# Kernel optimization log

Measured on AMD Instinct MI355X. Metric: run time of the kernel, lower is better.

Reference implementation:

```python
import jax, jax.numpy as jnp
import numpy as np

H = 1024
NH = 16
HD = H // NH
EPS = 1e-5

def setup_inputs() -> dict:
    key = jax.random.key(0)
    ks = jax.random.split(key, 5)
    B, S = 2, 2048
    scale = 1.0 / np.sqrt(H)
    return {
        "x": jax.random.normal(ks[0], (B, S, H), dtype=jnp.float32),
        "Wq": jax.random.normal(ks[1], (H, H), dtype=jnp.float32) * scale,
        "Wk": jax.random.normal(ks[2], (H, H), dtype=jnp.float32) * scale,
        "Wv": jax.random.normal(ks[3], (H, H), dtype=jnp.float32) * scale,
        "Wo": jax.random.normal(ks[4], (H, H), dtype=jnp.float32) * scale,
        "bo": jnp.zeros((H,), dtype=jnp.float32),
        "gamma": jnp.ones((H,), dtype=jnp.float32),
        "beta": jnp.zeros((H,), dtype=jnp.float32),
    }

def reference(x, Wq, Wk, Wv, Wo, bo, gamma, beta):
    B, S, _ = x.shape
    residual = x
    # pre-LayerNorm
    mu = jnp.mean(x, axis=-1, keepdims=True)
    var = jnp.mean(jnp.square(x - mu), axis=-1, keepdims=True)
    xn = (x - mu) * jax.lax.rsqrt(var + EPS) * gamma + beta
    # QKV projections (torch Linear: y = x @ W.T), split heads -> [B, NH, S, HD]
    q = (xn @ Wq.T).reshape(B, S, NH, HD).transpose(0, 2, 1, 3)
    k = (xn @ Wk.T).reshape(B, S, NH, HD).transpose(0, 2, 1, 3)
    v = (xn @ Wv.T).reshape(B, S, NH, HD).transpose(0, 2, 1, 3)
    # naive attention: explicit [B, NH, S, S] scores
    scale = 1.0 / np.sqrt(HD)
    scores = jnp.einsum('bhqd,bhkd->bhqk', q, k) * scale
    attn = jax.nn.softmax(scores.astype(jnp.float32), axis=-1).astype(q.dtype)
    out = jnp.einsum('bhqk,bhkd->bhqd', attn, v)
    out = out.transpose(0, 2, 1, 3).reshape(B, S, H)
    out = out @ Wo.T + bo
    return out + residual
```

## Files before the change

kernel.cpp:

```cpp
#include <hip/hip_runtime.h>
#include <hip/hip_bf16.h>

#define H 1024
#define NHEAD 16
#define HDIM 64
#define SEQ 2048
#define BATCH 2
#define M_TOT (BATCH * SEQ)
#define NQKV 3072

typedef __attribute__((ext_vector_type(8))) short bf16x8;
typedef __attribute__((ext_vector_type(4))) float f32x4;

#define C2_SCALE 0.18033688f

__device__ __forceinline__ unsigned short f2bf(float f) {
  union { float f; unsigned int u; } a;
  a.f = f;
  unsigned int u = a.u;
  return (unsigned short)((u + 0x7fffu + ((u >> 16) & 1u)) >> 16);
}

__device__ __forceinline__ unsigned int pkbf(float a, float b) {
  union { __hip_bfloat162 h; unsigned int u; } cv;
  cv.h = __float22bfloat162_rn(float2{a, b});
  return cv.u;
}

__device__ __forceinline__ float fast_exp2(float x) {
#if defined(__has_builtin) && __has_builtin(__builtin_amdgcn_exp2f)
  return __builtin_amdgcn_exp2f(x);
#else
  return exp2f(x);
#endif
}

typedef const __attribute__((address_space(1))) void* gas1_t;
typedef __attribute__((address_space(3))) void* las3_t;
__device__ __forceinline__ void gload16(const void* g, void* l) {
  __builtin_amdgcn_global_load_lds((gas1_t)(unsigned long long)g,
                                   (las3_t)(unsigned int)(unsigned long long)l,
                                   16, 0, 0);
}

__global__ __launch_bounds__(256) void ln_kernel(const float* __restrict__ x,
                                                 const float* __restrict__ gamma,
                                                 const float* __restrict__ beta,
                                                 unsigned short* __restrict__ xn) {
  const int row = blockIdx.x;
  const int t = threadIdx.x;
  const float* xr = x + (size_t)row * H;
  float4 v = ((const float4*)xr)[t];
  float s = v.x + v.y + v.z + v.w;
  float s2 = v.x * v.x + v.y * v.y + v.z * v.z + v.w * v.w;
#pragma unroll
  for (int o = 32; o; o >>= 1) {
    s += __shfl_xor(s, o, 64);
    s2 += __shfl_xor(s2, o, 64);
  }
  __shared__ float red[8];
  const int wave = t >> 6;
  if ((t & 63) == 0) {
    red[wave] = s;
    red[wave + 4] = s2;
  }
  __syncthreads();
  const float ts = red[0] + red[1] + red[2] + red[3];
  const float ts2 = red[4] + red[5] + red[6] + red[7];
  const float mu = ts * (1.0f / (float)H);
  const float var = ts2 * (1.0f / (float)H) - mu * mu;
  const float rstd = rsqrtf(var + 1e-5f);
  const float4 g = ((const float4*)gamma)[t];
  const float4 b = ((const float4*)beta)[t];
  ushort4 o;
  o.x = f2bf((v.x - mu) * rstd * g.x + b.x);
  o.y = f2bf((v.y - mu) * rstd * g.y + b.y);
  o.z = f2bf((v.z - mu) * rstd * g.z + b.z);
  o.w = f2bf((v.w - mu) * rstd * g.w + b.w);
  ((ushort4*)(xn + (size_t)row * H))[t] = o;
}

__global__ __launch_bounds__(256) void cast4_kernel(const float* __restrict__ s0,
                                                    const float* __restrict__ s1,
                                                    const float* __restrict__ s2,
                                                    const float* __restrict__ s3,
                                                    unsigned short* __restrict__ dst) {
  const int y = blockIdx.y;
  const float* s = (y == 0) ? s0 : (y == 1) ? s1 : (y == 2) ? s2 : s3;
  const int i = blockIdx.x * 256 + threadIdx.x;
  const float4 v = ((const float4*)s)[i];
  ushort4 o;
  o.x = f2bf(v.x);
  o.y = f2bf(v.y);
  o.z = f2bf(v.z);
  o.w = f2bf(v.w);
  ((ushort4*)(dst + (size_t)y * H * H))[i] = o;
}

template <int EPI>
__global__ __launch_bounds__(256) void gemm128(const unsigned short* __restrict__ A,
                                               const unsigned short* __restrict__ W,
                                               unsigned short* __restrict__ qk,
                                               unsigned short* __restrict__ vt,
                                               const float* __restrict__ bo,
                                               const float* __restrict__ x,
                                               float* __restrict__ out) {
  const int m0 = blockIdx.x * 128;
  const int n0 = blockIdx.y * 128;
  const int tid = threadIdx.x;
  const int wave = tid >> 6;
  const int lane = tid & 63;
  const int l16 = lane & 15;
  const int quad = lane >> 4;
  const int wx = wave & 1, wy = wave >> 1;

  __shared__ __align__(16) unsigned short As[128 * 32];
  __shared__ __align__(16) unsigned short Bs[128 * 32];

  const int sub = lane >> 2;
  const int kcol = (lane & 3) * 8;
  const unsigned short* ag = A + (size_t)(m0 + wave * 32 + sub) * H + kcol;
  const unsigned short* bg = W + (size_t)(n0 + wave * 32 + sub) * H + kcol;
  unsigned short* al = &As[wave * 32 * 32];
  unsigned short* bl = &Bs[wave * 32 * 32];

  f32x4 acc[4][4] = {};

  for (int k0 = 0; k0 < H; k0 += 32) {
    __syncthreads();
    gload16(ag + k0, al);
    gload16(ag + k0 + 16 * H, al + 16 * 32);
    gload16(bg + k0, bl);
    gload16(bg + k0 + 16 * H, bl + 16 * 32);
    __syncthreads();
    bf16x8 af[4], bf[4];
#pragma unroll
    for (int t = 0; t < 4; t++) {
      af[t] = *(const bf16x8*)&As[(wy * 64 + t * 16 + l16) * 32 + quad * 8];
      bf[t] = *(const bf16x8*)&Bs[(wx * 64 + t * 16 + l16) * 32 + quad * 8];
    }
#pragma unroll
    for (int i = 0; i < 4; i++)
#pragma unroll
      for (int j = 0; j < 4; j++)
        acc[i][j] = __builtin_amdgcn_mfma_f32_16x16x32_bf16(af[i], bf[j], acc[i][j], 0, 0, 0);
  }

  if (EPI == 0) {
#pragma unroll
    for (int j = 0; j < 4; j++) {
      const int cb = n0 + wx * 64 + j * 16;
      if (cb < 2048) {
        const float qs = (cb < 1024) ? C2_SCALE : 1.0f;
#pragma unroll
        for (int i = 0; i < 4; i++) {
          const int row = m0 + wy * 64 + i * 16 + quad * 4;
#pragma unroll
          for (int r = 0; r < 4; r++)
            qk[(size_t)(row + r) * 2048 + cb + l16] = f2bf(acc[i][j][r] * qs);
        }
      } else {
        const int n = cb + l16 - 2048;
#pragma unroll
        for (int i = 0; i < 4; i++) {
          const int row0 = m0 + wy * 64 + i * 16 + quad * 4;
          const int b = row0 >> 11;
          const int s = row0 & 2047;
          ushort4 p;
          p.x = f2bf(acc[i][j][0]);
          p.y = f2bf(acc[i][j][1]);
          p.z = f2bf(acc[i][j][2]);
          p.w = f2bf(acc[i][j][3]);
          *(ushort4*)&vt[((size_t)b * 1024 + n) * SEQ + s] = p;
        }
      }
    }
  } else {
#pragma unroll
    for (int j = 0; j < 4; j++) {
      const int col = n0 + wx * 64 + j * 16 + l16;
      const float bv = bo[col];
#pragma unroll
      for (int i = 0; i < 4; i++) {
        const int row = m0 + wy * 64 + i * 16 + quad * 4;
#pragma unroll
        for (int r = 0; r < 4; r++) {
          const size_t idx = (size_t)(row + r) * H + col;
          out[idx] = acc[i][j][r] + bv + x[idx];
        }
      }
    }
  }
}

__global__ __launch_bounds__(256, 4) void attn_kernel(const unsigned short* __restrict__ qk,
                                                      const unsigned short* __restrict__ vt,
                                                      unsigned short* __restrict__ O) {
  const int qt = blockIdx.x;
  const int h = blockIdx.y;
  const int b = blockIdx.z;
  const int tid = threadIdx.x;
  const int wave = tid >> 6;
  const int lane = tid & 63;
  const int l16 = lane & 15;
  const int quad = lane >> 4;
  const int l8 = l16 & 7;

  __shared__ __align__(16) unsigned short Kt[2][64 * 64];
  __shared__ __align__(16) unsigned short Vt[2][64 * 64];
  __shared__ __align__(16) unsigned short Pt[4][16 * 64];

  const unsigned short* Qbase = qk + (size_t)b * SEQ * 2048 + h * 64;
  const unsigned short* Kbase = qk + (size_t)b * SEQ * 2048 + 1024 + h * 64;
  const unsigned short* Vbase = vt + ((size_t)b * 1024 + h * 64) * SEQ;

  const int rIn = lane >> 3;
  const int gsw = (lane & 7) ^ rIn;
  const int ch0 = 2 * wave;

  const int qrow = qt * 64 + wave * 16 + l16;
  bf16x8 aq[2];
  aq[0] = *(const bf16x8*)(Qbase + (size_t)qrow * 2048 + quad * 8);
  aq[1] = *(const bf16x8*)(Qbase + (size_t)qrow * 2048 + 32 + quad * 8);

  float l_i = 0.0f;
  f32x4 o_acc[4] = {};

#pragma unroll
  for (int c = 0; c < 2; c++) {
    const int ch = ch0 + c;
    const int row = ch * 8 + rIn;
    gload16(Kbase + (size_t)row * 2048 + gsw * 8, &Kt[0][ch * 512]);
    gload16(Vbase + (size_t)row * SEQ + gsw * 8, &Vt[0][ch * 512]);
  }

  unsigned short* myP = &Pt[wave][0];

  for (int it = 0; it < SEQ / 64; it++) {
    const int bi = it & 1;
    __syncthreads();
    if (it + 1 < SEQ / 64) {
#pragma unroll
      for (int c = 0; c < 2; c++) {
        const int ch = ch0 + c;
        const int row = ch * 8 + rIn;
        gload16(Kbase + (size_t)((it + 1) * 64 + row) * 2048 + gsw * 8,
                &Kt[bi ^ 1][ch * 512]);
        gload16(Vbase + (size_t)row * SEQ + (it + 1) * 64 + gsw * 8,
                &Vt[bi ^ 1][ch * 512]);
      }
    }

    f32x4 s[4] = {};
#pragma unroll
    for (int c = 0; c < 2; c++) {
#pragma unroll
      for (int t = 0; t < 4; t++) {
        const bf16x8 kf =
            *(const bf16x8*)&Kt[bi][(t * 16 + l16) * 64 + (((c * 4 + quad) ^ l8) * 8)];
        s[t] = __builtin_amdgcn_mfma_f32_16x16x32_bf16(kf, aq[c], s[t], 0, 0, 0);
      }
    }

    float pv[4][4];
#pragma unroll
    for (int t = 0; t < 4; t++)
#pragma unroll
      for (int r = 0; r < 4; r++) {
        const float p = fast_exp2(s[t][r]);
        pv[t][r] = p;
        l_i += p;
      }

#pragma unroll
    for (int t = 0; t < 4; t++) {
      uint2 d;
      d.x = pkbf(pv[t][0], pv[t][1]);
      d.y = pkbf(pv[t][2], pv[t][3]);
      *(uint2*)&myP[l16 * 64 + (((t * 2 + (quad >> 1)) ^ l8) * 8) + (quad & 1) * 4] = d;
    }

#pragma unroll
    for (int c = 0; c < 2; c++) {
      const bf16x8 pb = *(const bf16x8*)&myP[l16 * 64 + (((c * 4 + quad) ^ l8) * 8)];
#pragma unroll
      for (int dt = 0; dt < 4; dt++) {
        const bf16x8 vf =
            *(const bf16x8*)&Vt[bi][(dt * 16 + l16) * 64 + (((c * 4 + quad) ^ l8) * 8)];
        o_acc[dt] = __builtin_amdgcn_mfma_f32_16x16x32_bf16(vf, pb, o_acc[dt], 0, 0, 0);
      }
    }
  }

  l_i += __shfl_xor(l_i, 16, 64);
  l_i += __shfl_xor(l_i, 32, 64);
  const float inv = 1.0f / l_i;
  unsigned short* orow = O + ((size_t)(b * SEQ + qrow)) * H + h * 64;
#pragma unroll
  for (int dt = 0; dt < 4; dt++) {
    uint2 d;
    d.x = pkbf(o_acc[dt][0] * inv, o_acc[dt][1] * inv);
    d.y = pkbf(o_acc[dt][2] * inv, o_acc[dt][3] * inv);
    *(uint2*)&orow[dt * 16 + quad * 4] = d;
  }
}

extern "C" void kernel_launch(void* const* d_in, const int* in_sizes, int n_in,
                              void* d_out, int out_size, void* d_ws, size_t ws_size,
                              hipStream_t stream) {
  const float* x = (const float*)d_in[0];
  const float* Wq = (const float*)d_in[1];
  const float* Wk = (const float*)d_in[2];
  const float* Wv = (const float*)d_in[3];
  const float* Wo = (const float*)d_in[4];
  const float* bo = (const float*)d_in[5];
  const float* gamma = (const float*)d_in[6];
  const float* beta = (const float*)d_in[7];
  float* out = (float*)d_out;

  unsigned short* ws = (unsigned short*)d_ws;
  unsigned short* xn = ws;
  unsigned short* wcat = xn + (size_t)M_TOT * H;
  unsigned short* wob = wcat + (size_t)3 * H * H;
  unsigned short* qkb = wcat + (size_t)4 * H * H;
  unsigned short* vtb = qkb + (size_t)M_TOT * 2048;
  unsigned short* atb = vtb + (size_t)BATCH * H * SEQ;

  ln_kernel<<<M_TOT, 256, 0, stream>>>(x, gamma, beta, xn);
  cast4_kernel<<<dim3(H * H / 1024, 4), 256, 0, stream>>>(Wq, Wk, Wv, Wo, wcat);
  gemm128<0><<<dim3(M_TOT / 128, NQKV / 128), 256, 0, stream>>>(
      xn, wcat, qkb, vtb, nullptr, nullptr, nullptr);
  attn_kernel<<<dim3(SEQ / 64, NHEAD, BATCH), 256, 0, stream>>>(qkb, vtb, atb);
  gemm128<1><<<dim3(M_TOT / 128, H / 128), 256, 0, stream>>>(
      atb, wob, nullptr, nullptr, bo, x, out);
}
```

Measured before the change: 210.5 us.

## Double-buffer GEMM LDS tiles and merge LayerNorm with weight cast

The GEMM's shared-memory tiles become two buffers. The next K-slice's global-to-LDS loads are issued before the MFMAs on the current slice, and only one barrier remains per iteration. This is meant to hide global load latency behind the matrix math. LDS use per block doubles, and the launch bound now asks for 4 blocks per SM. Separately, the LayerNorm and the four weight fp32-to-bf16 casts run in one combined launch, saving one kernel launch and letting the cast blocks fill idle compute units.

```diff
diff --git a/kernel.cpp b/kernel.cpp
--- a/kernel.cpp
+++ b/kernel.cpp
@@ -43,12 +43,31 @@
                                    16, 0, 0);
 }
 
-__global__ __launch_bounds__(256) void ln_kernel(const float* __restrict__ x,
-                                                 const float* __restrict__ gamma,
-                                                 const float* __restrict__ beta,
-                                                 unsigned short* __restrict__ xn) {
+__global__ __launch_bounds__(256) void ln_cast_kernel(const float* __restrict__ x,
+                                                      const float* __restrict__ gamma,
+                                                      const float* __restrict__ beta,
+                                                      unsigned short* __restrict__ xn,
+                                                      const float* __restrict__ w0,
+                                                      const float* __restrict__ w1,
+                                                      const float* __restrict__ w2,
+                                                      const float* __restrict__ w3,
+                                                      unsigned short* __restrict__ wdst) {
+  const int t = threadIdx.x;
+  if (blockIdx.x >= M_TOT) {
+    const int cb = blockIdx.x - M_TOT;
+    const int y = cb >> 10;
+    const float* s = (y == 0) ? w0 : (y == 1) ? w1 : (y == 2) ? w2 : w3;
+    const int i = (cb & 1023) * 256 + t;
+    const float4 v = ((const float4*)s)[i];
+    ushort4 o;
+    o.x = f2bf(v.x);
+    o.y = f2bf(v.y);
+    o.z = f2bf(v.z);
+    o.w = f2bf(v.w);
+    ((ushort4*)(wdst + (size_t)y * H * H))[i] = o;
+    return;
+  }
   const int row = blockIdx.x;
-  const int t = threadIdx.x;
   const float* xr = x + (size_t)row * H;
   float4 v = ((const float4*)xr)[t];
   float s = v.x + v.y + v.z + v.w;
@@ -80,31 +99,14 @@
   ((ushort4*)(xn + (size_t)row * H))[t] = o;
 }
 
-__global__ __launch_bounds__(256) void cast4_kernel(const float* __restrict__ s0,
-                                                    const float* __restrict__ s1,
-                                                    const float* __restrict__ s2,
-                                                    const float* __restrict__ s3,
-                                                    unsigned short* __restrict__ dst) {
-  const int y = blockIdx.y;
-  const float* s = (y == 0) ? s0 : (y == 1) ? s1 : (y == 2) ? s2 : s3;
-  const int i = blockIdx.x * 256 + threadIdx.x;
-  const float4 v = ((const float4*)s)[i];
-  ushort4 o;
-  o.x = f2bf(v.x);
-  o.y = f2bf(v.y);
-  o.z = f2bf(v.z);
-  o.w = f2bf(v.w);
-  ((ushort4*)(dst + (size_t)y * H * H))[i] = o;
-}
-
 template <int EPI>
-__global__ __launch_bounds__(256) void gemm128(const unsigned short* __restrict__ A,
-                                               const unsigned short* __restrict__ W,
-                                               unsigned short* __restrict__ qk,
-                                               unsigned short* __restrict__ vt,
-                                               const float* __restrict__ bo,
-                                               const float* __restrict__ x,
-                                               float* __restrict__ out) {
+__global__ __launch_bounds__(256, 4) void gemm128(const unsigned short* __restrict__ A,
+                                                  const unsigned short* __restrict__ W,
+                                                  unsigned short* __restrict__ qk,
+                                                  unsigned short* __restrict__ vt,
+                                                  const float* __restrict__ bo,
+                                                  const float* __restrict__ x,
+                                                  float* __restrict__ out) {
   const int m0 = blockIdx.x * 128;
   const int n0 = blockIdx.y * 128;
   const int tid = threadIdx.x;
@@ -114,30 +116,37 @@
   const int quad = lane >> 4;
   const int wx = wave & 1, wy = wave >> 1;
 
-  __shared__ __align__(16) unsigned short As[128 * 32];
-  __shared__ __align__(16) unsigned short Bs[128 * 32];
+  __shared__ __align__(16) unsigned short As[2][128 * 32];
+  __shared__ __align__(16) unsigned short Bs[2][128 * 32];
 
   const int sub = lane >> 2;
   const int kcol = (lane & 3) * 8;
   const unsigned short* ag = A + (size_t)(m0 + wave * 32 + sub) * H + kcol;
   const unsigned short* bg = W + (size_t)(n0 + wave * 32 + sub) * H + kcol;
-  unsigned short* al = &As[wave * 32 * 32];
-  unsigned short* bl = &Bs[wave * 32 * 32];
+  const int lofs = wave * 32 * 32;
 
   f32x4 acc[4][4] = {};
 
-  for (int k0 = 0; k0 < H; k0 += 32) {
+  gload16(ag, &As[0][lofs]);
+  gload16(ag + 16 * H, &As[0][lofs + 16 * 32]);
+  gload16(bg, &Bs[0][lofs]);
+  gload16(bg + 16 * H, &Bs[0][lofs + 16 * 32]);
+
+  for (int it = 0; it < H / 32; it++) {
+    const int bi = it & 1;
     __syncthreads();
-    gload16(ag + k0, al);
-    gload16(ag + k0 + 16 * H, al + 16 * 32);
-    gload16(bg + k0, bl);
-    gload16(bg + k0 + 16 * H, bl + 16 * 32);
-    __syncthreads();
+    if (it + 1 < H / 32) {
+      const int k1 = (it + 1) * 32;
+      gload16(ag + k1, &As[bi ^ 1][lofs]);
+      gload16(ag + k1 + 16 * H, &As[bi ^ 1][lofs + 16 * 32]);
+      gload16(bg + k1, &Bs[bi ^ 1][lofs]);
+      gload16(bg + k1 + 16 * H, &Bs[bi ^ 1][lofs + 16 * 32]);
+    }
     bf16x8 af[4], bf[4];
 #pragma unroll
     for (int t = 0; t < 4; t++) {
-      af[t] = *(const bf16x8*)&As[(wy * 64 + t * 16 + l16) * 32 + quad * 8];
-      bf[t] = *(const bf16x8*)&Bs[(wx * 64 + t * 16 + l16) * 32 + quad * 8];
+      af[t] = *(const bf16x8*)&As[bi][(wy * 64 + t * 16 + l16) * 32 + quad * 8];
+      bf[t] = *(const bf16x8*)&Bs[bi][(wx * 64 + t * 16 + l16) * 32 + quad * 8];
     }
 #pragma unroll
     for (int i = 0; i < 4; i++)
@@ -326,8 +335,8 @@
   unsigned short* vtb = qkb + (size_t)M_TOT * 2048;
   unsigned short* atb = vtb + (size_t)BATCH * H * SEQ;
 
-  ln_kernel<<<M_TOT, 256, 0, stream>>>(x, gamma, beta, xn);
-  cast4_kernel<<<dim3(H * H / 1024, 4), 256, 0, stream>>>(Wq, Wk, Wv, Wo, wcat);
+  ln_cast_kernel<<<M_TOT + 4096, 256, 0, stream>>>(x, gamma, beta, xn, Wq, Wk, Wv, Wo,
+                                                   wcat);
   gemm128<0><<<dim3(M_TOT / 128, NQKV / 128), 256, 0, stream>>>(
       xn, wcat, qkb, vtb, nullptr, nullptr, nullptr);
   attn_kernel<<<dim3(SEQ / 64, NHEAD, BATCH), 256, 0, stream>>>(qkb, vtb, atb);
```

Result: faster. 195.8 us (-7.0%).
